# Optimization experiments

Hardware: AMD Instinct MI355X
Metric: run time of the kernel (lower is better)

## Reference

```python
import jax, jax.numpy as jnp
import numpy as np

# 4-qubit statevector simulator (state shape (2,2,2,2)); RY and CNOT are real,
_CNOT = jnp.array([[1.,0.,0.,0.],[0.,1.,0.,0.],[0.,0.,0.,1.],[0.,0.,1.,0.]], dtype=jnp.float32).reshape(2,2,2,2)
_RING = [(0,1),(1,2),(2,3),(3,0)]

def _ry(state, theta, wire):
    h = 0.5 * theta
    c, s = jnp.cos(h), jnp.sin(h)
    m = jnp.stack([jnp.stack([c, -s]), jnp.stack([s, c])])
    return jnp.moveaxis(jnp.tensordot(m, state, axes=([1], [wire])), 0, wire)

def _cnot(state, c, t):
    out = jnp.tensordot(_CNOT, state, axes=([2, 3], [c, t]))
    return jnp.moveaxis(out, (0, 1), (c, t))

def _embed(x):
    # RY angle embedding of the flattened 2x2 patch onto 4 wires
    s = jnp.zeros((2, 2, 2, 2), dtype=x.dtype).at[0, 0, 0, 0].set(1.0)
    for i in range(4):
        s = _ry(s, x[i], i)
    return s

def _expz0(s):
    return jnp.sum(s[0] ** 2) - jnp.sum(s[1] ** 2)

def _circ_ran(x, w):   # 7 weights
    s = _embed(x)
    for i in range(4):
        s = _ry(s, w[i], i)
    s = _cnot(s, 0, 1); s = _cnot(s, 2, 3)
    s = _ry(s, w[4], 0); s = _ry(s, w[5], 2)
    s = _cnot(s, 1, 2)
    s = _ry(s, w[6], 1)
    return _expz0(s)

def _circ_line(x, w):  # 7 weights
    s = _embed(x)
    for i in range(4):
        s = _ry(s, w[i], i)
    for (c, t) in [(0, 1), (1, 2), (2, 3)]:
        s = _cnot(s, c, t)
    for i in range(3):
        s = _ry(s, w[4 + i], i + 1)
    return _expz0(s)

def _circ_ring(x, w):  # 8 weights
    s = _embed(x)
    for i in range(4):
        s = _ry(s, w[i], i)
    for (c, t) in _RING:
        s = _cnot(s, c, t)
    for i in range(4):
        s = _ry(s, w[4 + i], i)
    return _expz0(s)

def _circ_doublering(x, w):  # 16 weights: 2 layers x (4 RY + ring fwd + 4 RY + ring bwd)
    s = _embed(x)
    for L in range(2):
        b = 8 * L
        for i in range(4):
            s = _ry(s, w[b + i], i)
        for (c, t) in _RING:
            s = _cnot(s, c, t)
        for i in range(4):
            s = _ry(s, w[b + 4 + i], i)
        for (c, t) in reversed(_RING):
            s = _cnot(s, c, t)
    return _expz0(s)

def _circ_blockring(x, w):  # 12 weights: 3 layers x (4 RY + block+ring CNOTs)
    s = _embed(x)
    for L in range(3):
        for i in range(4):
            s = _ry(s, w[4 * L + i], i)
        for (c, t) in [(0, 1), (2, 3), (1, 2), (3, 0)]:
            s = _cnot(s, c, t)
    return _expz0(s)

_CIRCUITS = [(_circ_ran, 7), (_circ_line, 7), (_circ_ring, 8), (_circ_doublering, 16), (_circ_blockring, 12)]

def _forward(inputs, weights):
    B, C, H, W = inputs.shape
    Hp, Wp = H - 1, W - 1  # kernel_size=2, stride=1, no padding
    # sliding 2x2 patches, flattened row-major (matches reshape of [.., 2, 2] -> [.., 4])
    patches = jnp.stack([inputs[:, :, :Hp, :Wp], inputs[:, :, :Hp, 1:],
                         inputs[:, :, 1:, :Wp], inputs[:, :, 1:, 1:]], axis=-1)  # [B,C,Hp,Wp,4]
    x = jnp.moveaxis(patches, 1, 0).reshape(C, B * Hp * Wp, 4)  # [C, N, 4]
    O = weights.shape[0]
    outs = []
    for i in range(O):  # small structural loop: circuits differ by type i%5
        fn, nw = _CIRCUITS[i % 5]
        w = weights[i, :, :nw]  # [C, nw]
        per_c = jax.vmap(jax.vmap(fn, in_axes=(0, None)), in_axes=(0, 0))(x, w)  # [C, N]
        outs.append(per_c.sum(0))  # sum over input channels
    out = jnp.stack(outs, 0).reshape(O, B, Hp, Wp)
    return jnp.moveaxis(out, 0, 1)  # [B, O, Hp, Wp]

def setup_inputs() -> dict:
    key = jax.random.key(0)
    k1, k2 = jax.random.split(key)
    inputs = jax.random.normal(k1, (16, 3, 32, 32), dtype=jnp.float32)
    weights = jax.random.normal(k2, (16, 3, 16), dtype=jnp.float32)  # padded; circuit i uses first {7,7,8,16,12}[i%5]
    return {"inputs": inputs, "weights": weights}

def reference(inputs, weights):
    return _forward(inputs, weights)
```

## Files before the change

kernel.cpp:

```cpp
#include <hip/hip_runtime.h>


#define HPW 961
#define NPATCH 15376

template<int STRIDE>
__device__ __forceinline__ void ry_s(float* s, float c, float sn) {
#pragma unroll
    for (int i = 0; i < 16; ++i) {
        if ((i & STRIDE) == 0) {
            float a = s[i], b = s[i + STRIDE];
            s[i]          = c * a - sn * b;
            s[i + STRIDE] = sn * a + c * b;
        }
    }
}

template<int CS, int TS>
__device__ __forceinline__ void cnot_s(float* s) {
#pragma unroll
    for (int i = 0; i < 16; ++i) {
        if ((i & CS) != 0 && (i & TS) == 0) {
            float t = s[i]; s[i] = s[i + TS]; s[i + TS] = t;
        }
    }
}

__device__ __forceinline__ void build16(float* s,
        float c0, float s0, float c1, float s1,
        float c2, float s2, float c3, float s3) {
    const float m00 = c0 * c1, m01 = c0 * s1, m10 = s0 * c1, m11 = s0 * s1;
    const float n00 = c2 * c3, n01 = c2 * s3, n10 = s2 * c3, n11 = s2 * s3;
    s[0]  = m00 * n00; s[1]  = m00 * n01; s[2]  = m00 * n10; s[3]  = m00 * n11;
    s[4]  = m01 * n00; s[5]  = m01 * n01; s[6]  = m01 * n10; s[7]  = m01 * n11;
    s[8]  = m10 * n00; s[9]  = m10 * n01; s[10] = m10 * n10; s[11] = m10 * n11;
    s[12] = m11 * n00; s[13] = m11 * n01; s[14] = m11 * n10; s[15] = m11 * n11;
}

__device__ __forceinline__ float expz0v(const float* s) {
    float e = 0.0f;
#pragma unroll
    for (int i = 0; i < 8; ++i)  e += s[i] * s[i];
#pragma unroll
    for (int i = 8; i < 16; ++i) e -= s[i] * s[i];
    return e;
}

__global__ __launch_bounds__(256) void quanv_kernel(const float* __restrict__ in,
                                                    const float* __restrict__ wts,
                                                    float* __restrict__ out) {
    const int o = blockIdx.y;
    const int t = threadIdx.x;
    const int pidx = blockIdx.x * 256 + t;
    if (pidx >= NPATCH) return;
    const int b   = pidx / HPW;
    const int rem = pidx - b * HPW;
    const int h   = rem / 31;
    const int w   = rem - h * 31;
    const int circ = o % 5;

    const float* W  = wts + o * 48;
    const float* p0 = in + ((b * 3) * 32 + h) * 32 + w;
    float acc = 0.0f;

    switch (circ) {
    case 0: {
#pragma unroll
        for (int c = 0; c < 3; ++c) {
            const float* p  = p0 + c * 1024;
            const float* wc = W + c * 16;
            const float a0 = p[0] + wc[0];
            const float a1 = p[1] + wc[1];
            float s4, c4;  __sincosf(wc[4], &s4, &c4);
            float sa0, ca0; __sincosf(a0, &sa0, &ca0);
            const float sa1 = __sinf(a1);
            acc += c4 * ca0 - s4 * sa0 * sa1;
        }
    } break;
    case 1: {
#pragma unroll
        for (int c = 0; c < 3; ++c)
            acc += __cosf(p0[c * 1024] + W[c * 16]);
    } break;
    case 2: {
#pragma unroll
        for (int c = 0; c < 3; ++c) {
            const float* p  = p0 + c * 1024;
            const float* wc = W + c * 16;
            float c0,s0,c1,s1,c2,s2,c3,s3;
            __sincosf(0.5f * (p[0]  + wc[0]), &s0, &c0);
            __sincosf(0.5f * (p[1]  + wc[1]), &s1, &c1);
            __sincosf(0.5f * (p[32] + wc[2]), &s2, &c2);
            __sincosf(0.5f * (p[33] + wc[3]), &s3, &c3);
            float s[16]; build16(s, c0,s0,c1,s1,c2,s2,c3,s3);
            cnot_s<8,4>(s); cnot_s<4,2>(s); cnot_s<2,1>(s); cnot_s<1,8>(s);
            float sw, cw; __sincosf(0.5f * wc[4], &sw, &cw);
            ry_s<8>(s, cw, sw);
            acc += expz0v(s);
        }
    } break;
    case 3: {
#pragma unroll
        for (int c = 0; c < 3; ++c) {
            const float* p  = p0 + c * 1024;
            const float* wc = W + c * 16;
            float c0,s0,c1,s1,c2,s2,c3,s3;
            __sincosf(0.5f * (p[0]  + wc[0]), &s0, &c0);
            __sincosf(0.5f * (p[1]  + wc[1]), &s1, &c1);
            __sincosf(0.5f * (p[32] + wc[2]), &s2, &c2);
            __sincosf(0.5f * (p[33] + wc[3]), &s3, &c3);
            float s[16]; build16(s, c0,s0,c1,s1,c2,s2,c3,s3);
            cnot_s<8,4>(s); cnot_s<4,2>(s); cnot_s<2,1>(s); cnot_s<1,8>(s);
            float sg, cg;
            __sincosf(0.5f * wc[4], &sg, &cg); ry_s<8>(s, cg, sg);
            __sincosf(0.5f * wc[5], &sg, &cg); ry_s<4>(s, cg, sg);
            __sincosf(0.5f * wc[6], &sg, &cg); ry_s<2>(s, cg, sg);
            __sincosf(0.5f * wc[7], &sg, &cg); ry_s<1>(s, cg, sg);
            cnot_s<1,8>(s); cnot_s<2,1>(s); cnot_s<4,2>(s); cnot_s<8,4>(s);
            __sincosf(0.5f * wc[8],  &sg, &cg); ry_s<8>(s, cg, sg);
            __sincosf(0.5f * wc[9],  &sg, &cg); ry_s<4>(s, cg, sg);
            __sincosf(0.5f * wc[10], &sg, &cg); ry_s<2>(s, cg, sg);
            __sincosf(0.5f * wc[11], &sg, &cg); ry_s<1>(s, cg, sg);
            cnot_s<8,4>(s); cnot_s<4,2>(s); cnot_s<2,1>(s); cnot_s<1,8>(s);
            __sincosf(0.5f * wc[12], &sg, &cg); ry_s<8>(s, cg, sg);
            __sincosf(0.5f * wc[13], &sg, &cg); ry_s<4>(s, cg, sg);
            __sincosf(0.5f * wc[14], &sg, &cg); ry_s<2>(s, cg, sg);
            __sincosf(0.5f * wc[15], &sg, &cg); ry_s<1>(s, cg, sg);
            cnot_s<1,8>(s); cnot_s<2,1>(s); cnot_s<4,2>(s); cnot_s<8,4>(s);
            acc += expz0v(s);
        }
    } break;
    default: {
#pragma unroll
        for (int c = 0; c < 3; ++c) {
            const float* p  = p0 + c * 1024;
            const float* wc = W + c * 16;
            float c0,s0,c1,s1,c2,s2,c3,s3;
            __sincosf(0.5f * (p[0]  + wc[0]), &s0, &c0);
            __sincosf(0.5f * (p[1]  + wc[1]), &s1, &c1);
            __sincosf(0.5f * (p[32] + wc[2]), &s2, &c2);
            __sincosf(0.5f * (p[33] + wc[3]), &s3, &c3);
            float s[16]; build16(s, c0,s0,c1,s1,c2,s2,c3,s3);
            cnot_s<8,4>(s); cnot_s<2,1>(s); cnot_s<4,2>(s); cnot_s<1,8>(s);
            float sg, cg;
            __sincosf(0.5f * wc[4], &sg, &cg); ry_s<8>(s, cg, sg);
            __sincosf(0.5f * wc[5], &sg, &cg); ry_s<4>(s, cg, sg);
            __sincosf(0.5f * wc[6], &sg, &cg); ry_s<2>(s, cg, sg);
            __sincosf(0.5f * wc[7], &sg, &cg); ry_s<1>(s, cg, sg);
            cnot_s<8,4>(s); cnot_s<2,1>(s); cnot_s<4,2>(s); cnot_s<1,8>(s);
            __sincosf(0.5f * wc[8],  &sg, &cg); ry_s<8>(s, cg, sg);
            __sincosf(0.5f * wc[9],  &sg, &cg); ry_s<4>(s, cg, sg);
            __sincosf(0.5f * wc[10], &sg, &cg); ry_s<2>(s, cg, sg);
            __sincosf(0.5f * wc[11], &sg, &cg); ry_s<1>(s, cg, sg);
            cnot_s<8,4>(s); cnot_s<2,1>(s); cnot_s<4,2>(s); cnot_s<1,8>(s);
            acc += expz0v(s);
        }
    } break;
    }

    out[((b * 16 + o) * 31 + h) * 31 + w] = acc;
}

extern "C" void kernel_launch(void* const* d_in, const int* in_sizes, int n_in,
                              void* d_out, int out_size, void* d_ws, size_t ws_size,
                              hipStream_t stream) {
    const float* in  = (const float*)d_in[0];
    const float* wts = (const float*)d_in[1];
    float* out = (float*)d_out;
    dim3 grid((NPATCH + 255) / 256, 16);
    quanv_kernel<<<grid, 256, 0, stream>>>(in, wts, out);
}
```

Baseline: 61.77 us.

## Precompute weight rotations in LDS and prune gates not affecting <Z0>

Weight-only RY cos/sin pairs are computed once per block into shared memory instead of per thread. The circuit-2 (ring) case is replaced by a closed-form expectation, and trailing RY/CNOT gates that cannot change the wire-0 Z expectation are removed from the double-ring and block-ring cases. This cuts transcendental and state-update ALU work per patch, at the cost of a block-wide barrier and a small LDS table.

```diff
diff --git a/kernel.cpp b/kernel.cpp
--- a/kernel.cpp
+++ b/kernel.cpp
@@ -14,6 +14,11 @@
             s[i + STRIDE] = sn * a + c * b;
         }
     }
+}
+
+template<int STRIDE>
+__device__ __forceinline__ void ry_lds(float* s, float2 cs) {
+    ry_s<STRIDE>(s, cs.x, cs.y);
 }
 
 template<int CS, int TS>
@@ -40,17 +45,27 @@
 __device__ __forceinline__ float expz0v(const float* s) {
     float e = 0.0f;
 #pragma unroll
-    for (int i = 0; i < 8; ++i)  e += s[i] * s[i];
+    for (int i = 0; i < 8; ++i)  e = fmaf(s[i], s[i], e);
 #pragma unroll
-    for (int i = 8; i < 16; ++i) e -= s[i] * s[i];
+    for (int i = 8; i < 16; ++i) e = fmaf(-s[i], s[i], e);
     return e;
 }
 
 __global__ __launch_bounds__(256) void quanv_kernel(const float* __restrict__ in,
                                                     const float* __restrict__ wts,
                                                     float* __restrict__ out) {
+    __shared__ float2 wcs[48];
     const int o = blockIdx.y;
     const int t = threadIdx.x;
+    const float* W = wts + o * 48;
+
+    if (t < 48) {
+        float sn, cs;
+        __sincosf(0.5f * W[t], &sn, &cs);
+        wcs[t] = make_float2(cs, sn);
+    }
+    __syncthreads();
+
     const int pidx = blockIdx.x * 256 + t;
     if (pidx >= NPATCH) return;
     const int b   = pidx / HPW;
@@ -59,7 +74,6 @@
     const int w   = rem - h * 31;
     const int circ = o % 5;
 
-    const float* W  = wts + o * 48;
     const float* p0 = in + ((b * 3) * 32 + h) * 32 + w;
     float acc = 0.0f;
 
@@ -69,12 +83,12 @@
         for (int c = 0; c < 3; ++c) {
             const float* p  = p0 + c * 1024;
             const float* wc = W + c * 16;
-            const float a0 = p[0] + wc[0];
-            const float a1 = p[1] + wc[1];
-            float s4, c4;  __sincosf(wc[4], &s4, &c4);
-            float sa0, ca0; __sincosf(a0, &sa0, &ca0);
-            const float sa1 = __sinf(a1);
-            acc += c4 * ca0 - s4 * sa0 * sa1;
+            const float2 h4 = wcs[c * 16 + 4];
+            const float cf = fmaf(-2.0f * h4.y, h4.y, 1.0f);
+            const float sf = 2.0f * h4.x * h4.y;
+            float sa0, ca0; __sincosf(p[0] + wc[0], &sa0, &ca0);
+            const float sa1 = __sinf(p[1] + wc[1]);
+            acc += cf * ca0 - sf * sa0 * sa1;
         }
     } break;
     case 1: {
@@ -87,6 +101,22 @@
         for (int c = 0; c < 3; ++c) {
             const float* p  = p0 + c * 1024;
             const float* wc = W + c * 16;
+            const float2 h4 = wcs[c * 16 + 4];
+            const float cf = fmaf(-2.0f * h4.y, h4.y, 1.0f);
+            const float sf = 2.0f * h4.x * h4.y;
+            const float sa0 = __sinf(p[0] + wc[0]);
+            float sa1, ca1; __sincosf(p[1] + wc[1], &sa1, &ca1);
+            const float ca2 = __cosf(p[32] + wc[2]);
+            const float ca3 = __cosf(p[33] + wc[3]);
+            acc += cf * ca1 * ca2 * ca3 - sf * sa0 * sa1;
+        }
+    } break;
+    case 3: {
+#pragma unroll
+        for (int c = 0; c < 3; ++c) {
+            const float* p  = p0 + c * 1024;
+            const float* wc = W + c * 16;
+            const float2* g = wcs + c * 16;
             float c0,s0,c1,s1,c2,s2,c3,s3;
             __sincosf(0.5f * (p[0]  + wc[0]), &s0, &c0);
             __sincosf(0.5f * (p[1]  + wc[1]), &s1, &c1);
@@ -94,39 +124,12 @@
             __sincosf(0.5f * (p[33] + wc[3]), &s3, &c3);
             float s[16]; build16(s, c0,s0,c1,s1,c2,s2,c3,s3);
             cnot_s<8,4>(s); cnot_s<4,2>(s); cnot_s<2,1>(s); cnot_s<1,8>(s);
-            float sw, cw; __sincosf(0.5f * wc[4], &sw, &cw);
-            ry_s<8>(s, cw, sw);
-            acc += expz0v(s);
-        }
-    } break;
-    case 3: {
-#pragma unroll
-        for (int c = 0; c < 3; ++c) {
-            const float* p  = p0 + c * 1024;
-            const float* wc = W + c * 16;
-            float c0,s0,c1,s1,c2,s2,c3,s3;
-            __sincosf(0.5f * (p[0]  + wc[0]), &s0, &c0);
-            __sincosf(0.5f * (p[1]  + wc[1]), &s1, &c1);
-            __sincosf(0.5f * (p[32] + wc[2]), &s2, &c2);
-            __sincosf(0.5f * (p[33] + wc[3]), &s3, &c3);
-            float s[16]; build16(s, c0,s0,c1,s1,c2,s2,c3,s3);
+            ry_lds<8>(s, g[4]); ry_lds<4>(s, g[5]); ry_lds<2>(s, g[6]); ry_lds<1>(s, g[7]);
+            cnot_s<1,8>(s); cnot_s<2,1>(s); cnot_s<4,2>(s); cnot_s<8,4>(s);
+            ry_lds<8>(s, g[8]); ry_lds<4>(s, g[9]); ry_lds<2>(s, g[10]); ry_lds<1>(s, g[11]);
             cnot_s<8,4>(s); cnot_s<4,2>(s); cnot_s<2,1>(s); cnot_s<1,8>(s);
-            float sg, cg;
-            __sincosf(0.5f * wc[4], &sg, &cg); ry_s<8>(s, cg, sg);
-            __sincosf(0.5f * wc[5], &sg, &cg); ry_s<4>(s, cg, sg);
-            __sincosf(0.5f * wc[6], &sg, &cg); ry_s<2>(s, cg, sg);
-            __sincosf(0.5f * wc[7], &sg, &cg); ry_s<1>(s, cg, sg);
-            cnot_s<1,8>(s); cnot_s<2,1>(s); cnot_s<4,2>(s); cnot_s<8,4>(s);
-            __sincosf(0.5f * wc[8],  &sg, &cg); ry_s<8>(s, cg, sg);
-            __sincosf(0.5f * wc[9],  &sg, &cg); ry_s<4>(s, cg, sg);
-            __sincosf(0.5f * wc[10], &sg, &cg); ry_s<2>(s, cg, sg);
-            __sincosf(0.5f * wc[11], &sg, &cg); ry_s<1>(s, cg, sg);
-            cnot_s<8,4>(s); cnot_s<4,2>(s); cnot_s<2,1>(s); cnot_s<1,8>(s);
-            __sincosf(0.5f * wc[12], &sg, &cg); ry_s<8>(s, cg, sg);
-            __sincosf(0.5f * wc[13], &sg, &cg); ry_s<4>(s, cg, sg);
-            __sincosf(0.5f * wc[14], &sg, &cg); ry_s<2>(s, cg, sg);
-            __sincosf(0.5f * wc[15], &sg, &cg); ry_s<1>(s, cg, sg);
-            cnot_s<1,8>(s); cnot_s<2,1>(s); cnot_s<4,2>(s); cnot_s<8,4>(s);
+            ry_lds<8>(s, g[12]); ry_lds<1>(s, g[15]);
+            cnot_s<1,8>(s);
             acc += expz0v(s);
         }
     } break;
@@ -135,6 +138,7 @@
         for (int c = 0; c < 3; ++c) {
             const float* p  = p0 + c * 1024;
             const float* wc = W + c * 16;
+            const float2* g = wcs + c * 16;
             float c0,s0,c1,s1,c2,s2,c3,s3;
             __sincosf(0.5f * (p[0]  + wc[0]), &s0, &c0);
             __sincosf(0.5f * (p[1]  + wc[1]), &s1, &c1);
@@ -142,17 +146,10 @@
             __sincosf(0.5f * (p[33] + wc[3]), &s3, &c3);
             float s[16]; build16(s, c0,s0,c1,s1,c2,s2,c3,s3);
             cnot_s<8,4>(s); cnot_s<2,1>(s); cnot_s<4,2>(s); cnot_s<1,8>(s);
-            float sg, cg;
-            __sincosf(0.5f * wc[4], &sg, &cg); ry_s<8>(s, cg, sg);
-            __sincosf(0.5f * wc[5], &sg, &cg); ry_s<4>(s, cg, sg);
-            __sincosf(0.5f * wc[6], &sg, &cg); ry_s<2>(s, cg, sg);
-            __sincosf(0.5f * wc[7], &sg, &cg); ry_s<1>(s, cg, sg);
+            ry_lds<8>(s, g[4]); ry_lds<4>(s, g[5]); ry_lds<2>(s, g[6]); ry_lds<1>(s, g[7]);
             cnot_s<8,4>(s); cnot_s<2,1>(s); cnot_s<4,2>(s); cnot_s<1,8>(s);
-            __sincosf(0.5f * wc[8],  &sg, &cg); ry_s<8>(s, cg, sg);
-            __sincosf(0.5f * wc[9],  &sg, &cg); ry_s<4>(s, cg, sg);
-            __sincosf(0.5f * wc[10], &sg, &cg); ry_s<2>(s, cg, sg);
-            __sincosf(0.5f * wc[11], &sg, &cg); ry_s<1>(s, cg, sg);
-            cnot_s<8,4>(s); cnot_s<2,1>(s); cnot_s<4,2>(s); cnot_s<1,8>(s);
+            ry_lds<8>(s, g[8]); ry_lds<2>(s, g[10]); ry_lds<1>(s, g[11]);
+            cnot_s<2,1>(s); cnot_s<1,8>(s);
             acc += expz0v(s);
         }
     } break;
```

Measured after the change: 60.79 us. No clear change (-1.6%).
